# Performance work log

Hardware: AMD Instinct MI355X
Metric: run time of the kernel (lower is better)

The kernel has to match this reference:

```python
import jax, jax.numpy as jnp
import numpy as np

N_NODES = 1_000_000
N_EDGES = 16_000_000


def setup_inputs() -> dict:
    key = jax.random.key(0)
    ks = jax.random.split(key, 8)
    x = jax.random.normal(ks[0], (N_NODES, 9), dtype=jnp.float32)
    edge_index = jax.random.randint(ks[1], (2, N_EDGES), 0, N_NODES, dtype=jnp.int64)
    # Glorot-ish scaled params
    W1 = jax.random.normal(ks[2], (9, 16), dtype=jnp.float32) * 0.3
    b1 = jax.random.normal(ks[3], (16,), dtype=jnp.float32) * 0.01
    W2 = jax.random.normal(ks[4], (16, 10), dtype=jnp.float32) * 0.25
    b2 = jax.random.normal(ks[5], (10,), dtype=jnp.float32) * 0.01
    Wf = jax.random.normal(ks[6], (10, 1), dtype=jnp.float32) * 0.3
    bf = jax.random.normal(ks[7], (1,), dtype=jnp.float32) * 0.01
    return {"x": x, "edge_index": edge_index, "W1": W1, "b1": b1,
            "W2": W2, "b2": b2, "Wf": Wf, "bf": bf}


def _gcn_conv(x, W, b, row, col, norm, n):
    # PyG GCNConv: linear transform, then normalized scatter-add aggregation.
    h = x @ W                                   # [N, out]
    msg = h[row] * norm[:, None]                # gather + edgewise scale [E+N, out]
    out = jax.ops.segment_sum(msg, col, num_segments=n)  # scatter-add [N, out]
    return out + b


def reference(x, edge_index, W1, b1, W2, b2, Wf, bf):
    n = x.shape[0]
    # add self-loops (PyG default add_self_loops=True)
    loop = jnp.arange(n, dtype=edge_index.dtype)
    row = jnp.concatenate([edge_index[0], loop])
    col = jnp.concatenate([edge_index[1], loop])
    # symmetric normalization: deg computed over target nodes, weight 1 per edge
    deg = jax.ops.segment_sum(jnp.ones(row.shape[0], dtype=x.dtype), col,
                              num_segments=n)
    deg_inv_sqrt = jnp.where(deg > 0, jax.lax.rsqrt(jnp.maximum(deg, 1.0)), 0.0)
    norm = deg_inv_sqrt[row] * deg_inv_sqrt[col]  # [E+N]

    h = _gcn_conv(x, W1, b1, row, col, norm, n)
    h = jax.nn.relu(h)
    # dropout is identity in eval mode
    h = _gcn_conv(h, W2, b2, row, col, norm, n)
    return h @ Wf + bf
```

## Files before the change

kernel.cpp:

```cpp
#include <hip/hip_runtime.h>

static constexpr int NN = 1000000;
static constexpr int NE = 16000000;
static constexpr int BSH = 11;
static constexpr int BNODES = 1 << BSH;
static constexpr int BMASK = BNODES - 1;
static constexpr int NB = (NN + BMASK) >> BSH;
static constexpr int NWG = 512;
static constexpr int EPW = NE / NWG;
static constexpr int CHUNK = 16;
static constexpr int CAP = 24;
static constexpr int KE = 4;


__global__ __launch_bounds__(512) void k_count(const int* __restrict__ col,
                                               int* __restrict__ counts) {
    __shared__ int cnt[NB];
    for (int i = threadIdx.x; i < NB; i += 512) cnt[i] = 0;
    __syncthreads();
    long long e0 = (long long)blockIdx.x * EPW;
    long long e1 = e0 + EPW; if (e1 > NE) e1 = NE;
    long long e = e0 + threadIdx.x;
    for (; e + 3584 < e1; e += 4096) {
        int c0 = col[e],        c1 = col[e +  512];
        int c2 = col[e + 1024], c3 = col[e + 1536];
        int c4 = col[e + 2048], c5 = col[e + 2560];
        int c6 = col[e + 3072], c7 = col[e + 3584];
        atomicAdd(&cnt[c0 >> BSH], 1);
        atomicAdd(&cnt[c1 >> BSH], 1);
        atomicAdd(&cnt[c2 >> BSH], 1);
        atomicAdd(&cnt[c3 >> BSH], 1);
        atomicAdd(&cnt[c4 >> BSH], 1);
        atomicAdd(&cnt[c5 >> BSH], 1);
        atomicAdd(&cnt[c6 >> BSH], 1);
        atomicAdd(&cnt[c7 >> BSH], 1);
    }
    for (; e < e1; e += 512) atomicAdd(&cnt[col[e] >> BSH], 1);
    __syncthreads();
    int w = blockIdx.x;
    for (int i = threadIdx.x; i < NB; i += 512)
        counts[i * NWG + w] = cnt[i];
}


__global__ void k_scan_wg(int* __restrict__ counts, int* __restrict__ bucketTotal) {
    __shared__ int sm[NWG];
    int b = blockIdx.x, t = threadIdx.x;
    int v = counts[b * NWG + t];
    sm[t] = v;
    __syncthreads();
    for (int off = 1; off < NWG; off <<= 1) {
        int x = (t >= off) ? sm[t - off] : 0;
        __syncthreads();
        sm[t] += x;
        __syncthreads();
    }
    counts[b * NWG + t] = sm[t] - v;
    if (t == NWG - 1) bucketTotal[b] = sm[t];
}


__global__ void k_scan_total(const int* __restrict__ bucketTotal,
                             int* __restrict__ bucketBase, int* __restrict__ ptr) {
    __shared__ int sm[512];
    int t = threadIdx.x;
    int v = (t < NB) ? bucketTotal[t] : 0;
    sm[t] = v;
    __syncthreads();
    for (int off = 1; off < 512; off <<= 1) {
        int x = (t >= off) ? sm[t - off] : 0;
        __syncthreads();
        sm[t] += x;
        __syncthreads();
    }
    if (t < NB) bucketBase[t] = sm[t] - v;
    if (t == 0) { bucketBase[NB] = NE; ptr[NN] = NE; }
}


__global__ __launch_bounds__(512) void k_bin2(const int* __restrict__ row,
                                              const int* __restrict__ col,
                                              const int* __restrict__ counts,
                                              const int* __restrict__ bucketBase,
                                              unsigned* __restrict__ binned) {
    __shared__ unsigned stage[NB][CAP];
    __shared__ int scnt[NB];
    __shared__ int gcur[NB];
    int w = blockIdx.x;
    for (int i = threadIdx.x; i < NB; i += 512) {
        scnt[i] = 0;
        gcur[i] = bucketBase[i] + counts[i * NWG + w];
    }
    __syncthreads();
    long long e0 = (long long)w * EPW;
    long long e1 = e0 + EPW; if (e1 > NE) e1 = NE;
    const int TILE = 512 * KE;
    for (long long t0 = e0; t0 < e1; t0 += TILE) {
        int cs[KE], rs[KE];
        bool ok[KE];
#pragma unroll
        for (int k = 0; k < KE; ++k) {
            long long e = t0 + k * 512 + threadIdx.x;
            ok[k] = (e < e1);
            cs[k] = ok[k] ? col[e] : 0;
            rs[k] = ok[k] ? row[e] : 0;
        }
#pragma unroll
        for (int k = 0; k < KE; ++k) {
            if (ok[k]) {
                int b = cs[k] >> BSH;
                unsigned v = ((unsigned)rs[k] << BSH) | (unsigned)(cs[k] & BMASK);
                int s = atomicAdd(&scnt[b], 1);
                if (s < CAP) stage[b][s] = v;
                else { int p = atomicAdd(&gcur[b], 1); binned[p] = v; }
            }
        }
        __syncthreads();
        for (int b = threadIdx.x; b < NB; b += 512) {
            int n = scnt[b]; if (n > CAP) n = CAP;
            if (n >= CHUNK) {
                int p = atomicAdd(&gcur[b], CHUNK);
#pragma unroll
                for (int q = 0; q < CHUNK; ++q) binned[p + q] = stage[b][q];
                int rem = n - CHUNK;
                for (int q = 0; q < rem; ++q) stage[b][q] = stage[b][CHUNK + q];
                scnt[b] = rem;
            } else {
                scnt[b] = n;
            }
        }
        __syncthreads();
    }
    for (int b = threadIdx.x; b < NB; b += 512) {
        int n = scnt[b]; if (n > CAP) n = CAP;
        if (n > 0) {
            int p = atomicAdd(&gcur[b], n);
            for (int q = 0; q < n; ++q) binned[p + q] = stage[b][q];
        }
    }
}


__global__ __launch_bounds__(512) void k_sort(const unsigned* __restrict__ binned,
                                              const int* __restrict__ bucketBase,
                                              int* __restrict__ ptr,
                                              float* __restrict__ dis,
                                              int* __restrict__ sortedRow) {
    __shared__ int cnt[BNODES];
    __shared__ int tsum[512];
    int b = blockIdx.x, t = threadIdx.x;
    for (int i = t; i < BNODES; i += 512) cnt[i] = 0;
    __syncthreads();
    int i0 = bucketBase[b], i1 = bucketBase[b + 1];
    int i = i0 + t;
    for (; i + 3584 < i1; i += 4096) {
        unsigned v0 = binned[i],        v1 = binned[i +  512];
        unsigned v2 = binned[i + 1024], v3 = binned[i + 1536];
        unsigned v4 = binned[i + 2048], v5 = binned[i + 2560];
        unsigned v6 = binned[i + 3072], v7 = binned[i + 3584];
        atomicAdd(&cnt[v0 & BMASK], 1);
        atomicAdd(&cnt[v1 & BMASK], 1);
        atomicAdd(&cnt[v2 & BMASK], 1);
        atomicAdd(&cnt[v3 & BMASK], 1);
        atomicAdd(&cnt[v4 & BMASK], 1);
        atomicAdd(&cnt[v5 & BMASK], 1);
        atomicAdd(&cnt[v6 & BMASK], 1);
        atomicAdd(&cnt[v7 & BMASK], 1);
    }
    for (; i < i1; i += 512) atomicAdd(&cnt[binned[i] & BMASK], 1);
    __syncthreads();
    int s0 = cnt[t * 4], s1 = cnt[t * 4 + 1], s2 = cnt[t * 4 + 2], s3 = cnt[t * 4 + 3];
    int tot = s0 + s1 + s2 + s3;
    tsum[t] = tot;
    __syncthreads();
    for (int off = 1; off < 512; off <<= 1) {
        int x = (t >= off) ? tsum[t - off] : 0;
        __syncthreads();
        tsum[t] += x;
        __syncthreads();
    }
    int base = bucketBase[b] + tsum[t] - tot;
    int n0 = (b << BSH) + t * 4;
    if (n0 < NN)     { ptr[n0]     = base;                dis[n0]     = rsqrtf((float)(s0 + 1)); }
    if (n0 + 1 < NN) { ptr[n0 + 1] = base + s0;           dis[n0 + 1] = rsqrtf((float)(s1 + 1)); }
    if (n0 + 2 < NN) { ptr[n0 + 2] = base + s0 + s1;      dis[n0 + 2] = rsqrtf((float)(s2 + 1)); }
    if (n0 + 3 < NN) { ptr[n0 + 3] = base + s0 + s1 + s2; dis[n0 + 3] = rsqrtf((float)(s3 + 1)); }
    __syncthreads();
    cnt[t * 4]     = base;
    cnt[t * 4 + 1] = base + s0;
    cnt[t * 4 + 2] = base + s0 + s1;
    cnt[t * 4 + 3] = base + s0 + s1 + s2;
    __syncthreads();
    i = i0 + t;
    for (; i + 3584 < i1; i += 4096) {
        unsigned v0 = binned[i],        v1 = binned[i +  512];
        unsigned v2 = binned[i + 1024], v3 = binned[i + 1536];
        unsigned v4 = binned[i + 2048], v5 = binned[i + 2560];
        unsigned v6 = binned[i + 3072], v7 = binned[i + 3584];
        int p0 = atomicAdd(&cnt[v0 & BMASK], 1);
        int p1 = atomicAdd(&cnt[v1 & BMASK], 1);
        int p2 = atomicAdd(&cnt[v2 & BMASK], 1);
        int p3 = atomicAdd(&cnt[v3 & BMASK], 1);
        int p4 = atomicAdd(&cnt[v4 & BMASK], 1);
        int p5 = atomicAdd(&cnt[v5 & BMASK], 1);
        int p6 = atomicAdd(&cnt[v6 & BMASK], 1);
        int p7 = atomicAdd(&cnt[v7 & BMASK], 1);
        sortedRow[p0] = (int)(v0 >> BSH);
        sortedRow[p1] = (int)(v1 >> BSH);
        sortedRow[p2] = (int)(v2 >> BSH);
        sortedRow[p3] = (int)(v3 >> BSH);
        sortedRow[p4] = (int)(v4 >> BSH);
        sortedRow[p5] = (int)(v5 >> BSH);
        sortedRow[p6] = (int)(v6 >> BSH);
        sortedRow[p7] = (int)(v7 >> BSH);
    }
    for (; i < i1; i += 512) {
        unsigned v = binned[i];
        int pos = atomicAdd(&cnt[v & BMASK], 1);
        sortedRow[pos] = (int)(v >> BSH);
    }
}


__global__ void k_lin1(const float* __restrict__ x, const float* __restrict__ W1,
                       const float* __restrict__ dis, float* __restrict__ g1) {
    __shared__ float w[144];
    if (threadIdx.x < 144) w[threadIdx.x] = W1[threadIdx.x];
    __syncthreads();
    int i = blockIdx.x * blockDim.x + threadIdx.x;
    if (i >= NN) return;
    float xv[9];
#pragma unroll
    for (int k = 0; k < 9; ++k) xv[k] = x[(long long)i * 9 + k];
    float d = dis[i];
#pragma unroll
    for (int j = 0; j < 16; ++j) {
        float acc = 0.f;
#pragma unroll
        for (int k = 0; k < 9; ++k) acc = fmaf(xv[k], w[k * 16 + j], acc);
        g1[(long long)i * 16 + j] = acc * d;
    }
}


template <int MODE>
__global__ void k_pull_f(const int* __restrict__ ptr, const int* __restrict__ sortedRow,
                         const float* __restrict__ dis, const float* __restrict__ g,
                         const float* __restrict__ p0, const float* __restrict__ p1,
                         const float* __restrict__ p2, float* __restrict__ dst) {
    __shared__ float w2s[256];
    __shared__ float c16[16];
    __shared__ float wf16[16];
    __shared__ float bfs;
    if (MODE == 0) {
        if (threadIdx.x < 256) {
            int k = threadIdx.x >> 4, j = threadIdx.x & 15;
            w2s[threadIdx.x] = (j < 10) ? p1[k * 10 + j] : 0.f;
        }
        if (threadIdx.x < 16) c16[threadIdx.x] = p0[threadIdx.x];
    } else {
        if (threadIdx.x < 16) {
            c16[threadIdx.x]  = (threadIdx.x < 10) ? p0[threadIdx.x] : 0.f;
            wf16[threadIdx.x] = (threadIdx.x < 10) ? p1[threadIdx.x] : 0.f;
        }
        if (threadIdx.x == 0) bfs = p2[0];
    }
    __syncthreads();

    int grp = threadIdx.x >> 4;
    int j = threadIdx.x & 15;
    int n = blockIdx.x * 16 + grp;
    if (n >= NN) return;
    int e0 = ptr[n], e1 = ptr[n + 1];
    float acc = g[(long long)n * 16 + j];
    int e = e0;
    for (; e + 16 <= e1; e += 16) {
        int r[16];
#pragma unroll
        for (int k = 0; k < 16; ++k) r[k] = sortedRow[e + k];
        float v[16];
#pragma unroll
        for (int k = 0; k < 16; ++k) v[k] = g[(long long)r[k] * 16 + j];
        float s0 = ((v[0] + v[1]) + (v[2] + v[3])) + ((v[4] + v[5]) + (v[6] + v[7]));
        float s1 = ((v[8] + v[9]) + (v[10] + v[11])) + ((v[12] + v[13]) + (v[14] + v[15]));
        acc += s0 + s1;
    }
    for (; e + 4 <= e1; e += 4) {
        int r0 = sortedRow[e + 0], r1 = sortedRow[e + 1];
        int r2 = sortedRow[e + 2], r3 = sortedRow[e + 3];
        float v0 = g[(long long)r0 * 16 + j];
        float v1 = g[(long long)r1 * 16 + j];
        float v2 = g[(long long)r2 * 16 + j];
        float v3 = g[(long long)r3 * 16 + j];
        acc += (v0 + v1) + (v2 + v3);
    }
    for (; e < e1; ++e)
        acc += g[(long long)sortedRow[e] * 16 + j];

    float d = dis[n];
    float val = d * acc;
    if (MODE == 0) {
        float hv = fmaxf(val + c16[j], 0.f);
        float o = 0.f;
#pragma unroll
        for (int k = 0; k < 16; ++k)
            o = fmaf(__shfl(hv, k, 16), w2s[k * 16 + j], o);
        dst[(long long)n * 16 + j] = o * d;
    } else {
        float t = (val + c16[j]) * wf16[j];
#pragma unroll
        for (int m = 8; m >= 1; m >>= 1) t += __shfl_xor(t, m, 16);
        if (j == 0) dst[n] = t + bfs;
    }
}

extern "C" void kernel_launch(void* const* d_in, const int* in_sizes, int n_in,
                              void* d_out, int out_size, void* d_ws, size_t ws_size,
                              hipStream_t stream) {
    const float* x  = (const float*)d_in[0];
    const int*   ei = (const int*)d_in[1];
    const float* W1 = (const float*)d_in[2];
    const float* b1 = (const float*)d_in[3];
    const float* W2 = (const float*)d_in[4];
    const float* b2 = (const float*)d_in[5];
    const float* Wf = (const float*)d_in[6];
    const float* bf = (const float*)d_in[7];
    float* out = (float*)d_out;

    const int* row = ei;
    const int* col = ei + NE;

    char* ws = (char*)d_ws;
    size_t off = 0;
    auto alloc = [&](size_t bytes) -> void* {
        void* p = ws + off;
        off += (bytes + 255) & ~255ULL;
        return p;
    };
    int* counts      = (int*)alloc((size_t)NB * NWG * 4);
    int* bucketTotal = (int*)alloc((size_t)NB * 4);
    int* bucketBase  = (int*)alloc((size_t)(NB + 1) * 4);
    int* ptr         = (int*)alloc((size_t)(NN + 1) * 4);
    float* dis       = (float*)alloc((size_t)NN * 4);
    unsigned* binned = (unsigned*)alloc((size_t)NE * 4);
    int* sortedRow   = (int*)alloc((size_t)NE * 4);
    float* g1        = (float*)alloc((size_t)NN * 16 * 4);

    float* g2 = (float*)binned;

    const int TB = 256;
    const int nodeGrid = (NN + TB - 1) / TB;
    const int pullGrid = (NN + 15) / 16;

    k_count<<<NWG, 512, 0, stream>>>(col, counts);
    k_scan_wg<<<NB, NWG, 0, stream>>>(counts, bucketTotal);
    k_scan_total<<<1, 512, 0, stream>>>(bucketTotal, bucketBase, ptr);
    k_bin2<<<NWG, 512, 0, stream>>>(row, col, counts, bucketBase, binned);
    k_sort<<<NB, 512, 0, stream>>>(binned, bucketBase, ptr, dis, sortedRow);

    k_lin1<<<nodeGrid, TB, 0, stream>>>(x, W1, dis, g1);
    k_pull_f<0><<<pullGrid, TB, 0, stream>>>(ptr, sortedRow, dis, g1, b1, W2, nullptr, g2);
    k_pull_f<1><<<pullGrid, TB, 0, stream>>>(ptr, sortedRow, dis, g2, b2, Wf, bf, out);
}
```

Baseline: 905.7 us.

## Vectorize edge loads, replicate LDS histograms, and stage lin1 inputs via shared memory

Changes the workgroup count to 500 so each group's edge range divides evenly into int4 loads, then reads col/row as int4 in both k_count and k_bin2. k_count now keeps four replicated LDS histograms to reduce atomic contention. k_lin1 stages x through shared memory using coalesced float4 loads and writes g1 as float4. The scan kernel is padded to 512 threads to handle the non-power-of-two group count. The cost targeted is uncoalesced scalar memory traffic and LDS atomic conflicts; the trade-off is fewer, larger workgroups and a little extra LDS.

```diff
diff --git a/kernel.cpp b/kernel.cpp
--- a/kernel.cpp
+++ b/kernel.cpp
@@ -6,57 +6,49 @@
 static constexpr int BNODES = 1 << BSH;
 static constexpr int BMASK = BNODES - 1;
 static constexpr int NB = (NN + BMASK) >> BSH;
-static constexpr int NWG = 512;
+static constexpr int NWG = 500;
 static constexpr int EPW = NE / NWG;
 static constexpr int CHUNK = 16;
 static constexpr int CAP = 24;
-static constexpr int KE = 4;
 
 
 __global__ __launch_bounds__(512) void k_count(const int* __restrict__ col,
                                                int* __restrict__ counts) {
-    __shared__ int cnt[NB];
-    for (int i = threadIdx.x; i < NB; i += 512) cnt[i] = 0;
-    __syncthreads();
-    long long e0 = (long long)blockIdx.x * EPW;
-    long long e1 = e0 + EPW; if (e1 > NE) e1 = NE;
-    long long e = e0 + threadIdx.x;
-    for (; e + 3584 < e1; e += 4096) {
-        int c0 = col[e],        c1 = col[e +  512];
-        int c2 = col[e + 1024], c3 = col[e + 1536];
-        int c4 = col[e + 2048], c5 = col[e + 2560];
-        int c6 = col[e + 3072], c7 = col[e + 3584];
-        atomicAdd(&cnt[c0 >> BSH], 1);
-        atomicAdd(&cnt[c1 >> BSH], 1);
-        atomicAdd(&cnt[c2 >> BSH], 1);
-        atomicAdd(&cnt[c3 >> BSH], 1);
-        atomicAdd(&cnt[c4 >> BSH], 1);
-        atomicAdd(&cnt[c5 >> BSH], 1);
-        atomicAdd(&cnt[c6 >> BSH], 1);
-        atomicAdd(&cnt[c7 >> BSH], 1);
-    }
-    for (; e < e1; e += 512) atomicAdd(&cnt[col[e] >> BSH], 1);
+    __shared__ int cnt[4][NB];
+    for (int i = threadIdx.x; i < 4 * NB; i += 512) ((int*)cnt)[i] = 0;
     __syncthreads();
     int w = blockIdx.x;
+    int rep = threadIdx.x & 3;
+    const int4* col4 = (const int4*)(col + (long long)w * EPW);
+    const int nq = EPW / 4;
+    for (int q = threadIdx.x; q < nq; q += 512) {
+        int4 c = col4[q];
+        atomicAdd(&cnt[rep][c.x >> BSH], 1);
+        atomicAdd(&cnt[rep][c.y >> BSH], 1);
+        atomicAdd(&cnt[rep][c.z >> BSH], 1);
+        atomicAdd(&cnt[rep][c.w >> BSH], 1);
+    }
+    __syncthreads();
     for (int i = threadIdx.x; i < NB; i += 512)
-        counts[i * NWG + w] = cnt[i];
-}
-
-
-__global__ void k_scan_wg(int* __restrict__ counts, int* __restrict__ bucketTotal) {
-    __shared__ int sm[NWG];
+        counts[i * NWG + w] = cnt[0][i] + cnt[1][i] + cnt[2][i] + cnt[3][i];
+}
+
+
+__global__ __launch_bounds__(512) void k_scan_wg(int* __restrict__ counts,
+                                                 int* __restrict__ bucketTotal) {
+    __shared__ int sm[512];
     int b = blockIdx.x, t = threadIdx.x;
-    int v = counts[b * NWG + t];
+    int v = (t < NWG) ? counts[b * NWG + t] : 0;
     sm[t] = v;
     __syncthreads();
-    for (int off = 1; off < NWG; off <<= 1) {
+    for (int off = 1; off < 512; off <<= 1) {
         int x = (t >= off) ? sm[t - off] : 0;
         __syncthreads();
         sm[t] += x;
         __syncthreads();
     }
-    counts[b * NWG + t] = sm[t] - v;
-    if (t == NWG - 1) bucketTotal[b] = sm[t];
+    if (t < NWG) counts[b * NWG + t] = sm[t] - v;
+    if (t == 511) bucketTotal[b] = sm[511];
 }
 
 
@@ -92,24 +84,21 @@
         gcur[i] = bucketBase[i] + counts[i * NWG + w];
     }
     __syncthreads();
-    long long e0 = (long long)w * EPW;
-    long long e1 = e0 + EPW; if (e1 > NE) e1 = NE;
-    const int TILE = 512 * KE;
-    for (long long t0 = e0; t0 < e1; t0 += TILE) {
-        int cs[KE], rs[KE];
-        bool ok[KE];
-#pragma unroll
-        for (int k = 0; k < KE; ++k) {
-            long long e = t0 + k * 512 + threadIdx.x;
-            ok[k] = (e < e1);
-            cs[k] = ok[k] ? col[e] : 0;
-            rs[k] = ok[k] ? row[e] : 0;
-        }
-#pragma unroll
-        for (int k = 0; k < KE; ++k) {
-            if (ok[k]) {
-                int b = cs[k] >> BSH;
-                unsigned v = ((unsigned)rs[k] << BSH) | (unsigned)(cs[k] & BMASK);
+    const int4* col4 = (const int4*)(col + (long long)w * EPW);
+    const int4* row4 = (const int4*)(row + (long long)w * EPW);
+    const int nq = EPW / 4;
+    for (int q0 = 0; q0 < nq; q0 += 512) {
+        int q = q0 + threadIdx.x;
+        int4 c, r;
+        bool ok = (q < nq);
+        if (ok) { c = col4[q]; r = row4[q]; }
+        if (ok) {
+            int cc[4] = {c.x, c.y, c.z, c.w};
+            int rr[4] = {r.x, r.y, r.z, r.w};
+#pragma unroll
+            for (int k = 0; k < 4; ++k) {
+                int b = cc[k] >> BSH;
+                unsigned v = ((unsigned)rr[k] << BSH) | (unsigned)(cc[k] & BMASK);
                 int s = atomicAdd(&scnt[b], 1);
                 if (s < CAP) stage[b][s] = v;
                 else { int p = atomicAdd(&gcur[b], 1); binned[p] = v; }
@@ -121,9 +110,9 @@
             if (n >= CHUNK) {
                 int p = atomicAdd(&gcur[b], CHUNK);
 #pragma unroll
-                for (int q = 0; q < CHUNK; ++q) binned[p + q] = stage[b][q];
+                for (int t = 0; t < CHUNK; ++t) binned[p + t] = stage[b][t];
                 int rem = n - CHUNK;
-                for (int q = 0; q < rem; ++q) stage[b][q] = stage[b][CHUNK + q];
+                for (int t = 0; t < rem; ++t) stage[b][t] = stage[b][CHUNK + t];
                 scnt[b] = rem;
             } else {
                 scnt[b] = n;
@@ -135,7 +124,7 @@
         int n = scnt[b]; if (n > CAP) n = CAP;
         if (n > 0) {
             int p = atomicAdd(&gcur[b], n);
-            for (int q = 0; q < n; ++q) binned[p + q] = stage[b][q];
+            for (int t = 0; t < n; ++t) binned[p + t] = stage[b][t];
         }
     }
 }
@@ -222,24 +211,42 @@
 }
 
 
-__global__ void k_lin1(const float* __restrict__ x, const float* __restrict__ W1,
-                       const float* __restrict__ dis, float* __restrict__ g1) {
+__global__ __launch_bounds__(256) void k_lin1(const float* __restrict__ x,
+                                              const float* __restrict__ W1,
+                                              const float* __restrict__ dis,
+                                              float* __restrict__ g1) {
     __shared__ float w[144];
-    if (threadIdx.x < 144) w[threadIdx.x] = W1[threadIdx.x];
-    __syncthreads();
-    int i = blockIdx.x * blockDim.x + threadIdx.x;
-    if (i >= NN) return;
-    float xv[9];
-#pragma unroll
-    for (int k = 0; k < 9; ++k) xv[k] = x[(long long)i * 9 + k];
-    float d = dis[i];
+    __shared__ float xs[2304];
+    int t = threadIdx.x;
+    if (t < 144) w[t] = W1[t];
+    long long f4base = (long long)blockIdx.x * 576;
+    const float4* xv = (const float4*)x;
+#pragma unroll
+    for (int i = 0; i < 3; ++i) {
+        int idx = t + i * 256;
+        if (idx < 576 && f4base + idx < (long long)NN * 9 / 4)
+            ((float4*)xs)[idx] = xv[f4base + idx];
+    }
+    __syncthreads();
+    int n = blockIdx.x * 256 + t;
+    if (n >= NN) return;
+    float xvr[9];
+#pragma unroll
+    for (int k = 0; k < 9; ++k) xvr[k] = xs[t * 9 + k];
+    float d = dis[n];
+    float o[16];
 #pragma unroll
     for (int j = 0; j < 16; ++j) {
         float acc = 0.f;
 #pragma unroll
-        for (int k = 0; k < 9; ++k) acc = fmaf(xv[k], w[k * 16 + j], acc);
-        g1[(long long)i * 16 + j] = acc * d;
-    }
+        for (int k = 0; k < 9; ++k) acc = fmaf(xvr[k], w[k * 16 + j], acc);
+        o[j] = acc * d;
+    }
+    float4* dst = (float4*)(g1 + (long long)n * 16);
+    dst[0] = make_float4(o[0], o[1], o[2], o[3]);
+    dst[1] = make_float4(o[4], o[5], o[6], o[7]);
+    dst[2] = make_float4(o[8], o[9], o[10], o[11]);
+    dst[3] = make_float4(o[12], o[13], o[14], o[15]);
 }
 
 
@@ -353,7 +360,7 @@
     const int pullGrid = (NN + 15) / 16;
 
     k_count<<<NWG, 512, 0, stream>>>(col, counts);
-    k_scan_wg<<<NB, NWG, 0, stream>>>(counts, bucketTotal);
+    k_scan_wg<<<NB, 512, 0, stream>>>(counts, bucketTotal);
     k_scan_total<<<1, 512, 0, stream>>>(bucketTotal, bucketBase, ptr);
     k_bin2<<<NWG, 512, 0, stream>>>(row, col, counts, bucketBase, binned);
     k_sort<<<NB, 512, 0, stream>>>(binned, bucketBase, ptr, dis, sortedRow);
```

Result: faster. 876.7 us (median of 2 runs) (-3.2%).
